# Optimization experiments

Measured on AMD Instinct MI355X. Metric: run time of the kernel, lower is better.

Reference implementation:

```python
import jax, jax.numpy as jnp
import numpy as np

K_WIN = 3  # fixed kernel width in the original module
PAD = (K_WIN - 1) // 2


def setup_inputs() -> dict:
    key = jax.random.key(0)
    k1, k2, k3 = jax.random.split(key, 3)
    B, L, D, T = 32, 2048, 256, 64
    x = jax.random.normal(k1, (B, L, D), dtype=jnp.float32)
    C = jax.random.normal(k2, (T, D), dtype=jnp.float32) * (1.0 / np.sqrt(D))
    W_den = jax.random.normal(k3, (D, K_WIN * D), dtype=jnp.float32) * (1.0 / np.sqrt(D))
    b_den = jnp.zeros((K_WIN * D,), dtype=jnp.float32)
    return {"x": x, "C": C, "W_den": W_den, "b_den": b_den}


def reference(x, C, W_den, b_den):
    B, L, D = x.shape
    T = C.shape[0]
    # kc = relu(C @ W + b): [T, k*D] -> [T, k, D]
    kc = jax.nn.relu(C @ W_den + b_den).reshape(T, K_WIN, D)
    # att = x @ C^T: [B, L, T]
    att = jnp.einsum('bld,td->blt', x, C)
    # per-position dynamic kernels: [B, L, k, D]
    ki = jnp.einsum('blt,tkd->blkd', att, kc)
    # sliding windows of padded x: [B, L, k, D]
    x_pad = jnp.pad(x, ((0, 0), (PAD, PAD), (0, 0)))
    windows = jnp.stack([x_pad[:, j:j + L, :] for j in range(K_WIN)], axis=2)
    # windowed multiply-sum over k: [B, L, D]
    return jnp.sum(windows * ki, axis=2)
```

## Files before the change

### kernel.cpp

```cpp
#include <hip/hip_runtime.h>

#define B_  32
#define L_  2048
#define D_  256
#define T_  64
#define KW  3

typedef float f32x4 __attribute__((ext_vector_type(4)));
typedef short s16x8 __attribute__((ext_vector_type(8)));
typedef short s16x4 __attribute__((ext_vector_type(4)));

__device__ __forceinline__ short f2bf(float f) {
    unsigned u = __builtin_bit_cast(unsigned, f);
    u += 0x7FFFu + ((u >> 16) & 1u);
    return (short)(u >> 16);
}

__global__ __launch_bounds__(256) void prep_kernel(const float* __restrict__ C,
                                                   const float* __restrict__ W,
                                                   const float* __restrict__ bias,
                                                   short* __restrict__ CbfPk,
                                                   short* __restrict__ kcPk) {
    __shared__ float Ws[256 * 16];
    const int tid = threadIdx.x;

    if (blockIdx.x < 16) {
        const int i0 = (blockIdx.x * 256 + tid) * 4;
        const int t = i0 >> 8, d = i0 & 255;
        const f32x4 v = *(const f32x4*)(C + i0);
        s16x4 s;
        s[0] = f2bf(v[0]); s[1] = f2bf(v[1]); s[2] = f2bf(v[2]); s[3] = f2bf(v[3]);
        const int tt = t >> 4, c = t & 15, ks = d >> 5, gg = (d >> 3) & 3, e = d & 7;
        *(s16x4*)&CbfPk[(((tt * 8 + ks) * 4 + gg) * 16 + c) * 8 + e] = s;
        return;
    }

    const int nb = blockIdx.x - 16;
    const int n0 = nb * 16;

    for (int idx = tid; idx < 256 * 16; idx += 256) {
        const int dd = idx >> 4, nl = idx & 15;
        Ws[idx] = W[dd * (KW * D_) + n0 + nl];
    }
    __syncthreads();

    const int t  = tid >> 2;
    const int nl = tid & 3;
    float acc[4];
    #pragma unroll
    for (int i = 0; i < 4; ++i) acc[i] = bias[n0 + nl + 4 * i];

    const float* Crow = C + t * D_;
    for (int dd = 0; dd < D_; ++dd) {
        const float cv = Crow[dd];
        #pragma unroll
        for (int i = 0; i < 4; ++i)
            acc[i] = fmaf(cv, Ws[dd * 16 + nl + 4 * i], acc[i]);
    }
    const int ks = t >> 5, gg = (t >> 3) & 3, e = t & 7;
    #pragma unroll
    for (int i = 0; i < 4; ++i) {
        const int cc = nl + 4 * i;
        kcPk[(((nb * 2 + ks) * 4 + gg) * 16 + cc) * 8 + e] = f2bf(fmaxf(acc[i], 0.f));
    }
}

#define XSTF 268
#define ATS 72

__device__ __forceinline__ s16x8 cvt8(const float* p) {
    s16x8 r;
    #pragma unroll
    for (int i = 0; i < 8; ++i) r[i] = f2bf(p[i]);
    return r;
}

__global__ __launch_bounds__(256, 8) void main_kernel(const float* __restrict__ x,
                                                      const short* __restrict__ CbfPk,
                                                      const short* __restrict__ kcPk,
                                                      float* __restrict__ out) {
    __shared__ float xsf[18 * XSTF];
    __shared__ short atts[16 * ATS];

    const int tid  = threadIdx.x;
    const int w    = tid >> 6;
    const int lane = tid & 63;
    const int c    = lane & 15;
    const int g    = lane >> 4;
    const int l0   = blockIdx.x * 16;
    const int b    = blockIdx.y;

    const float* xb = x + (size_t)b * L_ * D_;

    #pragma unroll
    for (int k = 0; k < 5; ++k) {
        const int row = w + k * 4;
        if (row < 18) {
            const int l = l0 - 1 + row;
            float* ldsrow = &xsf[row * XSTF];
            if (l >= 0 && l < L_) {
                const float* gsrc = xb + (size_t)l * D_ + lane * 4;
                __builtin_amdgcn_global_load_lds(
                    (const __attribute__((address_space(1))) void*)gsrc,
                    (__attribute__((address_space(3))) void*)ldsrow,
                    16, 0, 0);
            } else {
                *(f32x4*)&ldsrow[lane * 4] = (f32x4){0.f, 0.f, 0.f, 0.f};
            }
        }
    }
    __syncthreads();

    {
        f32x4 acc = (f32x4){0.f, 0.f, 0.f, 0.f};
        const float* xr = &xsf[(1 + c) * XSTF];
        #pragma unroll
        for (int ks = 0; ks < 8; ++ks) {
            const s16x8 cb = *(const s16x8*)&CbfPk[(((w * 8 + ks) * 4 + g) * 16 + c) * 8];
            const s16x8 a  = cvt8(&xr[ks * 32 + g * 8]);
            acc = __builtin_amdgcn_mfma_f32_16x16x32_bf16(a, cb, acc, 0, 0, 0);
        }
        #pragma unroll
        for (int r = 0; r < 4; ++r)
            atts[(g * 4 + r) * ATS + w * 16 + c] = f2bf(acc[r]);
    }
    __syncthreads();

    const s16x8 afr0 = *(const s16x8*)&atts[c * ATS + 0 * 32 + g * 8];
    const s16x8 afr1 = *(const s16x8*)&atts[c * ATS + 1 * 32 + g * 8];

    const size_t outBase = ((size_t)b * L_ + l0) * D_;

    #pragma unroll
    for (int dtl = 0; dtl < 4; ++dtl) {
        const int dcol = w * 64 + dtl * 16 + c;
        const int nbb  = w * 4 + dtl;
        const s16x8 b0 = *(const s16x8*)&kcPk[((((0 * 16 + nbb) * 2 + 0) * 4 + g) * 16 + c) * 8];
        const s16x8 b1 = *(const s16x8*)&kcPk[((((0 * 16 + nbb) * 2 + 1) * 4 + g) * 16 + c) * 8];
        const s16x8 b2 = *(const s16x8*)&kcPk[((((1 * 16 + nbb) * 2 + 0) * 4 + g) * 16 + c) * 8];
        const s16x8 b3 = *(const s16x8*)&kcPk[((((1 * 16 + nbb) * 2 + 1) * 4 + g) * 16 + c) * 8];
        const s16x8 b4 = *(const s16x8*)&kcPk[((((2 * 16 + nbb) * 2 + 0) * 4 + g) * 16 + c) * 8];
        const s16x8 b5 = *(const s16x8*)&kcPk[((((2 * 16 + nbb) * 2 + 1) * 4 + g) * 16 + c) * 8];

        f32x4 a0 = (f32x4){0.f,0.f,0.f,0.f};
        f32x4 a1 = (f32x4){0.f,0.f,0.f,0.f};
        f32x4 a2 = (f32x4){0.f,0.f,0.f,0.f};
        a0 = __builtin_amdgcn_mfma_f32_16x16x32_bf16(afr0, b0, a0, 0, 0, 0);
        a0 = __builtin_amdgcn_mfma_f32_16x16x32_bf16(afr1, b1, a0, 0, 0, 0);
        a1 = __builtin_amdgcn_mfma_f32_16x16x32_bf16(afr0, b2, a1, 0, 0, 0);
        a1 = __builtin_amdgcn_mfma_f32_16x16x32_bf16(afr1, b3, a1, 0, 0, 0);
        a2 = __builtin_amdgcn_mfma_f32_16x16x32_bf16(afr0, b4, a2, 0, 0, 0);
        a2 = __builtin_amdgcn_mfma_f32_16x16x32_bf16(afr1, b5, a2, 0, 0, 0);

        float xv[6];
        #pragma unroll
        for (int i = 0; i < 6; ++i)
            xv[i] = xsf[(g * 4 + i) * XSTF + dcol];

        #pragma unroll
        for (int r = 0; r < 4; ++r) {
            const float o = a0[r] * xv[r] + a1[r] * xv[r + 1] + a2[r] * xv[r + 2];
            out[outBase + (size_t)(g * 4 + r) * D_ + dcol] = o;
        }
    }
}

extern "C" void kernel_launch(void* const* d_in, const int* in_sizes, int n_in,
                              void* d_out, int out_size, void* d_ws, size_t ws_size,
                              hipStream_t stream) {
    const float* x    = (const float*)d_in[0];
    const float* C    = (const float*)d_in[1];
    const float* Wden = (const float*)d_in[2];
    const float* bden = (const float*)d_in[3];
    float* out = (float*)d_out;

    short* kcPk  = (short*)d_ws;
    short* CbfPk = (short*)d_ws + KW * D_ * T_;

    prep_kernel<<<dim3(64), dim3(256), 0, stream>>>(C, Wden, bden, CbfPk, kcPk);

    dim3 grid(L_ / 16, B_);
    main_kernel<<<grid, dim3(256), 0, stream>>>(x, CbfPk, kcPk, out);
}
```

Measured before the change: 49.09 us.

## Split attention projection into separate kernel and process 32-row tiles

Splits the fused main kernel in two. The first kernel computes att = x·C^T in bf16 for 32-row tiles and writes it to workspace in MFMA-fragment order. The second kernel reloads x in fp32, reads the packed att fragments and applies the dynamic-kernel MFMAs and the windowed sum over 32 rows per block. This is meant to remove the in-LDS fp32-to-bf16 conversion and the extra barrier from the main path and to raise work per block. The cost is reading x twice from global memory, an extra launch, and a workspace round trip for att.

```diff
diff --git a/kernel.cpp b/kernel.cpp
--- a/kernel.cpp
+++ b/kernel.cpp
@@ -65,69 +65,107 @@
     }
 }
 
-#define XSTF 268
-#define ATS 72
-
-__device__ __forceinline__ s16x8 cvt8(const float* p) {
-    s16x8 r;
-    #pragma unroll
-    for (int i = 0; i < 8; ++i) r[i] = f2bf(p[i]);
-    return r;
-}
-
-__global__ __launch_bounds__(256, 8) void main_kernel(const float* __restrict__ x,
-                                                      const short* __restrict__ CbfPk,
-                                                      const short* __restrict__ kcPk,
-                                                      float* __restrict__ out) {
-    __shared__ float xsf[18 * XSTF];
-    __shared__ short atts[16 * ATS];
+#define K1XST 264
+#define K1ATS 72
+
+__global__ __launch_bounds__(256, 7) void att_kernel(const float* __restrict__ x,
+                                                     const short* __restrict__ CbfPk,
+                                                     short* __restrict__ attPk) {
+    __shared__ short xs[32 * K1XST];
+    __shared__ short atts[32 * K1ATS];
 
     const int tid  = threadIdx.x;
     const int w    = tid >> 6;
     const int lane = tid & 63;
     const int c    = lane & 15;
     const int g    = lane >> 4;
-    const int l0   = blockIdx.x * 16;
+    const int l0   = blockIdx.x * 32;
     const int b    = blockIdx.y;
 
-    const float* xb = x + (size_t)b * L_ * D_;
-
-    #pragma unroll
-    for (int k = 0; k < 5; ++k) {
-        const int row = w + k * 4;
-        if (row < 18) {
-            const int l = l0 - 1 + row;
-            float* ldsrow = &xsf[row * XSTF];
-            if (l >= 0 && l < L_) {
-                const float* gsrc = xb + (size_t)l * D_ + lane * 4;
-                __builtin_amdgcn_global_load_lds(
-                    (const __attribute__((address_space(1))) void*)gsrc,
-                    (__attribute__((address_space(3))) void*)ldsrow,
-                    16, 0, 0);
-            } else {
-                *(f32x4*)&ldsrow[lane * 4] = (f32x4){0.f, 0.f, 0.f, 0.f};
-            }
-        }
+    const f32x4* x4 = (const f32x4*)(x + (size_t)b * L_ * D_);
+    #pragma unroll
+    for (int k = 0; k < 8; ++k) {
+        const int idx = tid + k * 256;
+        const int row = idx >> 6;
+        const int d4  = idx & 63;
+        const f32x4 v = x4[(size_t)(l0 + row) * 64 + d4];
+        s16x4 s;
+        s[0] = f2bf(v[0]); s[1] = f2bf(v[1]); s[2] = f2bf(v[2]); s[3] = f2bf(v[3]);
+        *(s16x4*)&xs[row * K1XST + d4 * 4] = s;
     }
     __syncthreads();
 
     {
-        f32x4 acc = (f32x4){0.f, 0.f, 0.f, 0.f};
-        const float* xr = &xsf[(1 + c) * XSTF];
+        const int m  = w & 1;
+        const int tp = w >> 1;
+        f32x4 acc0 = (f32x4){0.f, 0.f, 0.f, 0.f};
+        f32x4 acc1 = (f32x4){0.f, 0.f, 0.f, 0.f};
+        const short* xr = &xs[(m * 16 + c) * K1XST];
         #pragma unroll
         for (int ks = 0; ks < 8; ++ks) {
-            const s16x8 cb = *(const s16x8*)&CbfPk[(((w * 8 + ks) * 4 + g) * 16 + c) * 8];
-            const s16x8 a  = cvt8(&xr[ks * 32 + g * 8]);
-            acc = __builtin_amdgcn_mfma_f32_16x16x32_bf16(a, cb, acc, 0, 0, 0);
-        }
-        #pragma unroll
-        for (int r = 0; r < 4; ++r)
-            atts[(g * 4 + r) * ATS + w * 16 + c] = f2bf(acc[r]);
-    }
-    __syncthreads();
-
-    const s16x8 afr0 = *(const s16x8*)&atts[c * ATS + 0 * 32 + g * 8];
-    const s16x8 afr1 = *(const s16x8*)&atts[c * ATS + 1 * 32 + g * 8];
+            const s16x8 a   = *(const s16x8*)&xr[ks * 32 + g * 8];
+            const s16x8 cb0 = *(const s16x8*)&CbfPk[((((tp * 2 + 0) * 8 + ks) * 4 + g) * 16 + c) * 8];
+            const s16x8 cb1 = *(const s16x8*)&CbfPk[((((tp * 2 + 1) * 8 + ks) * 4 + g) * 16 + c) * 8];
+            acc0 = __builtin_amdgcn_mfma_f32_16x16x32_bf16(a, cb0, acc0, 0, 0, 0);
+            acc1 = __builtin_amdgcn_mfma_f32_16x16x32_bf16(a, cb1, acc1, 0, 0, 0);
+        }
+        #pragma unroll
+        for (int r = 0; r < 4; ++r) {
+            atts[(m * 16 + g * 4 + r) * K1ATS + (tp * 2 + 0) * 16 + c] = f2bf(acc0[r]);
+            atts[(m * 16 + g * 4 + r) * K1ATS + (tp * 2 + 1) * 16 + c] = f2bf(acc1[r]);
+        }
+    }
+    __syncthreads();
+
+    {
+        const int pm = tid >> 7;
+        const int ck = tid & 127;
+        const int q  = ck >> 6;
+        const int ln = ck & 63;
+        const int g2 = ln >> 4;
+        const int c2 = ln & 15;
+        const s16x8 v = *(const s16x8*)&atts[(pm * 16 + c2) * K1ATS + q * 32 + g2 * 8];
+        const size_t tile = (size_t)b * (L_ / 16) + blockIdx.x * 2 + pm;
+        *(s16x8*)&attPk[tile * 1024 + ck * 8] = v;
+    }
+}
+
+#define XSF 260
+
+__global__ __launch_bounds__(256, 4) void main2_kernel(const float* __restrict__ x,
+                                                       const short* __restrict__ attPk,
+                                                       const short* __restrict__ kcPk,
+                                                       float* __restrict__ out) {
+    __shared__ float xsf[34 * XSF];
+
+    const int tid  = threadIdx.x;
+    const int w    = tid >> 6;
+    const int lane = tid & 63;
+    const int c    = lane & 15;
+    const int g    = lane >> 4;
+    const int l0   = blockIdx.x * 32;
+    const int b    = blockIdx.y;
+
+    const size_t t0 = ((size_t)b * (L_ / 16) + blockIdx.x * 2) * 1024;
+    const s16x8 am00 = *(const s16x8*)&attPk[t0 + (0 * 64 + lane) * 8];
+    const s16x8 am01 = *(const s16x8*)&attPk[t0 + (1 * 64 + lane) * 8];
+    const s16x8 am10 = *(const s16x8*)&attPk[t0 + 1024 + (0 * 64 + lane) * 8];
+    const s16x8 am11 = *(const s16x8*)&attPk[t0 + 1024 + (1 * 64 + lane) * 8];
+
+    const f32x4* x4 = (const f32x4*)(x + (size_t)b * L_ * D_);
+    #pragma unroll
+    for (int k = 0; k < 9; ++k) {
+        const int idx = tid + k * 256;
+        if (idx < 34 * 64) {
+            const int row = idx >> 6;
+            const int d4  = idx & 63;
+            const int l   = l0 - 1 + row;
+            f32x4 v = (l >= 0 && l < L_) ? x4[(size_t)l * 64 + d4]
+                                         : (f32x4){0.f, 0.f, 0.f, 0.f};
+            *(f32x4*)&xsf[row * XSF + d4 * 4] = v;
+        }
+    }
+    __syncthreads();
 
     const size_t outBase = ((size_t)b * L_ + l0) * D_;
 
@@ -142,25 +180,30 @@
         const s16x8 b4 = *(const s16x8*)&kcPk[((((2 * 16 + nbb) * 2 + 0) * 4 + g) * 16 + c) * 8];
         const s16x8 b5 = *(const s16x8*)&kcPk[((((2 * 16 + nbb) * 2 + 1) * 4 + g) * 16 + c) * 8];
 
-        f32x4 a0 = (f32x4){0.f,0.f,0.f,0.f};
-        f32x4 a1 = (f32x4){0.f,0.f,0.f,0.f};
-        f32x4 a2 = (f32x4){0.f,0.f,0.f,0.f};
-        a0 = __builtin_amdgcn_mfma_f32_16x16x32_bf16(afr0, b0, a0, 0, 0, 0);
-        a0 = __builtin_amdgcn_mfma_f32_16x16x32_bf16(afr1, b1, a0, 0, 0, 0);
-        a1 = __builtin_amdgcn_mfma_f32_16x16x32_bf16(afr0, b2, a1, 0, 0, 0);
-        a1 = __builtin_amdgcn_mfma_f32_16x16x32_bf16(afr1, b3, a1, 0, 0, 0);
-        a2 = __builtin_amdgcn_mfma_f32_16x16x32_bf16(afr0, b4, a2, 0, 0, 0);
-        a2 = __builtin_amdgcn_mfma_f32_16x16x32_bf16(afr1, b5, a2, 0, 0, 0);
-
-        float xv[6];
-        #pragma unroll
-        for (int i = 0; i < 6; ++i)
-            xv[i] = xsf[(g * 4 + i) * XSTF + dcol];
-
-        #pragma unroll
-        for (int r = 0; r < 4; ++r) {
-            const float o = a0[r] * xv[r] + a1[r] * xv[r + 1] + a2[r] * xv[r + 2];
-            out[outBase + (size_t)(g * 4 + r) * D_ + dcol] = o;
+        #pragma unroll
+        for (int m = 0; m < 2; ++m) {
+            const s16x8 af0 = m ? am10 : am00;
+            const s16x8 af1 = m ? am11 : am01;
+            f32x4 a0 = (f32x4){0.f,0.f,0.f,0.f};
+            f32x4 a1 = (f32x4){0.f,0.f,0.f,0.f};
+            f32x4 a2 = (f32x4){0.f,0.f,0.f,0.f};
+            a0 = __builtin_amdgcn_mfma_f32_16x16x32_bf16(af0, b0, a0, 0, 0, 0);
+            a0 = __builtin_amdgcn_mfma_f32_16x16x32_bf16(af1, b1, a0, 0, 0, 0);
+            a1 = __builtin_amdgcn_mfma_f32_16x16x32_bf16(af0, b2, a1, 0, 0, 0);
+            a1 = __builtin_amdgcn_mfma_f32_16x16x32_bf16(af1, b3, a1, 0, 0, 0);
+            a2 = __builtin_amdgcn_mfma_f32_16x16x32_bf16(af0, b4, a2, 0, 0, 0);
+            a2 = __builtin_amdgcn_mfma_f32_16x16x32_bf16(af1, b5, a2, 0, 0, 0);
+
+            float xv[6];
+            #pragma unroll
+            for (int i = 0; i < 6; ++i)
+                xv[i] = xsf[(m * 16 + g * 4 + i) * XSF + dcol];
+
+            #pragma unroll
+            for (int r = 0; r < 4; ++r) {
+                const float o = a0[r] * xv[r] + a1[r] * xv[r + 1] + a2[r] * xv[r + 2];
+                out[outBase + (size_t)(m * 16 + g * 4 + r) * D_ + dcol] = o;
+            }
         }
     }
 }
@@ -176,9 +219,11 @@
 
     short* kcPk  = (short*)d_ws;
     short* CbfPk = (short*)d_ws + KW * D_ * T_;
+    short* attPk = CbfPk + T_ * D_;
 
     prep_kernel<<<dim3(64), dim3(256), 0, stream>>>(C, Wden, bden, CbfPk, kcPk);
 
-    dim3 grid(L_ / 16, B_);
-    main_kernel<<<grid, dim3(256), 0, stream>>>(x, CbfPk, kcPk, out);
-}
+    att_kernel<<<dim3(L_ / 32, B_), dim3(256), 0, stream>>>(x, CbfPk, attPk);
+
+    main2_kernel<<<dim3(L_ / 32, B_), dim3(256), 0, stream>>>(x, attPk, kcPk, out);
+}
```

Result: slower. 64.21 us (+30.8%).
